# Optimization experiments

Measured on AMD Instinct MI355X. Metric: run time of the kernel, lower is better.

The kernel has to match this reference:

```python
import jax, jax.numpy as jnp
import numpy as np
from jax import lax

B_CAPS, C_CAPS, K, STRIDE, ITERS = 32, 32, 3, 2, 3
BATCH, WIN = 8, 14
W_OUT = (WIN - K) // STRIDE + 1  # 6
CWW = C_CAPS * W_OUT * W_OUT     # 1152
LOG_2PI = float(np.log(2.0 * np.pi))


def setup_inputs() -> dict:
    key = jax.random.key(0)
    k1, k2, k3, k4, k5 = jax.random.split(key, 5)
    return {
        "poses": jax.random.normal(k1, (BATCH, B_CAPS, WIN, WIN, 16), jnp.float32),
        "activations": jax.random.uniform(k2, (BATCH, B_CAPS, WIN, WIN), jnp.float32),
        "lambda_": jnp.ones((), jnp.float32),
        "W": jax.random.normal(k3, (B_CAPS, K, K, C_CAPS, 4, 4), jnp.float32),
        "beta_v": jax.random.normal(k4, (1, CWW, 1), jnp.float32),
        "beta_a": jax.random.normal(k5, (1, CWW), jnp.float32),
    }


def reference(poses, activations, lambda_, W, beta_v, beta_a):
    b, B, win = poses.shape[0], poses.shape[1], poses.shape[2]
    C = W.shape[3]
    w = (win - K) // STRIDE + 1
    Bkk, Cww = B * K * K, C * w * w

    pose = poses.reshape(b, 16, B, win, win).transpose(0, 2, 3, 4, 1)

    # im2col patch extraction (vectorized): rows[i,k] = stride*i + k
    rows = ((jnp.arange(w) * STRIDE)[:, None] + jnp.arange(K)).reshape(-1)  # (w*K,)
    p = jnp.take(pose, rows, axis=2).reshape(b, B, w, K, win, 16)
    p = jnp.take(p, rows, axis=4).reshape(b, B, w, K, w, K, 16)
    patches = p.transpose(0, 1, 3, 5, 6, 2, 4)          # (b,B,K,K,16,wi,wj)
    # faithful reproduction of torch's view (b,B,K,K,16,ww)->(b,B,K,K,1,w,w,4,4)
    patches = patches.reshape(b, B, K, K, w, w, 4, 4)

    # votes: broadcast 4x4 matmul W @ pose-patch
    votes = jnp.einsum('sxyzij,bsxyuvjk->bsxyzuvik', W, patches)
    votes = votes.reshape(b, Bkk, Cww, 16)

    # activation patches, tiled over C (coordinate_add=False branch)
    a = jnp.take(activations, rows, axis=2).reshape(b, B, w, K, win)
    a = jnp.take(a, rows, axis=4).reshape(b, B, w, K, w, K)
    a = a.transpose(0, 1, 3, 5, 2, 4).reshape(b, Bkk, 1, w * w)
    act = jnp.broadcast_to(a, (b, Bkk, C, w * w)).reshape(b, Bkk, Cww)

    # EM routing
    R = jnp.ones((b, Bkk, Cww), votes.dtype) / Cww
    for i in range(ITERS + 1):
        Ra = (R * act)[..., None]                        # (b,Bkk,Cww,1)
        sum_R = Ra.sum(1)                                # (b,Cww,1)
        mu = ((Ra * votes).sum(1) / sum_R)[:, None]      # (b,1,Cww,16)
        sigma_sq = (Ra * (votes - mu) ** 2).sum(1) / sum_R  # (b,Cww,16)
        if i != ITERS:
            mu_d = lax.stop_gradient(mu)
            ss_d = lax.stop_gradient(sigma_sq)[:, None]  # (b,1,Cww,16)
            V_d = lax.stop_gradient(votes)
            a_d = lax.stop_gradient(act)
            log_p = -0.5 * (V_d - mu_d) ** 2 / ss_d - 0.5 * jnp.log(ss_d) - 0.5 * LOG_2PI
            ap = a_d * jnp.exp(log_p).sum(-1)            # (b,Bkk,Cww)
            R = ap / ap.sum(-1, keepdims=True)
        else:
            cost = (beta_v + jnp.log(sigma_sq)) * sum_R  # (b,Cww,16)
            a_out = jax.nn.sigmoid(lambda_ * (beta_a - cost.sum(2)))  # (b,Cww)

    return (mu.reshape(b, C, w, w, 16), a_out.reshape(b, C, w, w))
```

## Files before the change

kernel.cpp:

```cpp
#include <hip/hip_runtime.h>
#include <hip/hip_bf16.h>

#define NB   8
#define NM   288
#define NN   1152
#define NUV  36
#define ND   16

#define OFF_P    0
#define SZ_P     (NB*NUV*NM*ND)
#define OFF_WT   (OFF_P + SZ_P)
#define SZ_WT    (32*NM*ND)
#define OFF_ACT  (OFF_WT + SZ_WT)
#define SZ_ACT   (NB*NUV*NM)
#define OFF_L    (OFF_ACT + SZ_ACT)
#define SZ_L     (NB*NN*NM)
#define OFF_LSE  (OFF_L + SZ_L)
#define SZ_LSE   (NB*NM)
#define OFF_FLAG (OFF_LSE + SZ_LSE)
#define OFF_PM   (OFF_FLAG + 16)
#define SZ_PM    (NB*NUV*NM)
#define OFF_PS   (OFF_PM + SZ_PM)
#define SZ_PS    (NB*NUV*NM)

#define HALF_LOG_2PI 0.9189385332046727f
#define LOG_NN       7.049254841255839f
#define NEG_BIG      (-1.0e30f)

__device__ __forceinline__ float ldin(const void* p, int i, int f32) {
    return f32 ? ((const float*)p)[i]
               : __bfloat162float(((const __hip_bfloat16*)p)[i]);
}

__device__ __forceinline__ unsigned short bfbits(float f) {
    __hip_bfloat16 h = __float2bfloat16(f);
    return __builtin_bit_cast(unsigned short, h);
}

__device__ __forceinline__ float dot2bf(unsigned a, unsigned b, float c) {
    float d;
    asm("v_dot2_f32_bf16 %0, %1, %2, %3" : "=v"(d) : "v"(a), "v"(b), "v"(c));
    return d;
}

__device__ __forceinline__ int sniff(const unsigned short* u16) {
    int wild = 0;
    for (int i = 0; i < 64; ++i) {
        int ex = (u16[i] >> 7) & 0xFF;
        if (ex >= 133) ++wild;
    }
    return (wild >= 4) ? 1 : 0;
}

__global__ __launch_bounds__(256) void prep_kernel(
    const void* __restrict__ poses, const void* __restrict__ acts,
    const void* __restrict__ Wb, __hip_bfloat16* __restrict__ P,
    __hip_bfloat16* __restrict__ Wt, float* __restrict__ A36,
    int* __restrict__ flagw)
{
    const int blk = blockIdx.x;
    const int tid = threadIdx.x;
    __shared__ int lflag;
    if (tid == 0) {
        int f = sniff((const unsigned short*)poses);
        lflag = f;
        if (blk == 0) *flagw = f;
    }
    __syncthreads();
    const int f32 = lflag;

    if (blk < 256) {
        __shared__ float ps[16 * 196];
        __shared__ float asld[196];
        const int b = blk >> 5, s = blk & 31;
        for (int e = tid; e < 16 * 196; e += 256) {
            int c = e / 196, hw = e % 196;
            ps[e] = ldin(poses, ((b * 16 + c) * 32 + s) * 196 + hw, f32);
        }
        for (int e = tid; e < 196; e += 256)
            asld[e] = ldin(acts, (b * 32 + s) * 196 + e, f32);
        __syncthreads();
        for (int o2 = tid; o2 < 648; o2 += 256) {
            int row = o2 >> 1, half = o2 & 1;
            int uv = row / 9, xy = row % 9;
            int u = uv / 6, vv2 = uv % 6;
            int x = xy / 3, y = xy % 3;
            unsigned pk[4];
#pragma unroll
            for (int h = 0; h < 4; ++h) {
                unsigned lohi[2];
#pragma unroll
                for (int e = 0; e < 2; ++e) {
                    int kj = half * 8 + h * 2 + e;
                    int k = kj >> 2, j = kj & 3;
                    int idx = u * 96 + vv2 * 16 + j * 4 + k;
                    int c = idx / 36, rem = idx % 36;
                    int wi = rem / 6, wj = rem % 6;
                    lohi[e] = bfbits(ps[c * 196 + (2 * wi + x) * 14 + (2 * wj + y)]);
                }
                pk[h] = lohi[0] | (lohi[1] << 16);
            }
            *((uint4*)(P + (((size_t)((b * 36 + uv) * 288 + s * 9 + xy)) << 4) + half * 8)) =
                make_uint4(pk[0], pk[1], pk[2], pk[3]);
        }
        for (int o = tid; o < 324; o += 256) {
            int uv = o / 9, xy = o % 9;
            int u = uv / 6, vv2 = uv % 6;
            int x = xy / 3, y = xy % 3;
            A36[(b * 36 + uv) * 288 + s * 9 + xy] =
                __logf(asld[(2 * u + x) * 14 + (2 * vv2 + y)]);
        }
    } else {
        int idx = (blk - 256) * 256 + tid;
        int z = idx / 288, m = idx % 288;
        unsigned pk[8];
#pragma unroll
        for (int h = 0; h < 8; ++h) {
            unsigned lo = bfbits(ldin(Wb, m * 512 + z * 16 + 2 * h, f32));
            unsigned hi = bfbits(ldin(Wb, m * 512 + z * 16 + 2 * h + 1, f32));
            pk[h] = lo | (hi << 16);
        }
        uint4* dst = (uint4*)(Wt + idx * 16);
        dst[0] = make_uint4(pk[0], pk[1], pk[2], pk[3]);
        dst[1] = make_uint4(pk[4], pk[5], pk[6], pk[7]);
    }
}

__global__ __launch_bounds__(288, 4) void em_iter(
    const unsigned short* __restrict__ wsP, const unsigned short* __restrict__ wsWt,
    const float* __restrict__ wsA, float* __restrict__ wsL,
    const float* __restrict__ wsLSE,
    const void* __restrict__ beta_v,
    const void* __restrict__ beta_a,
    const void* __restrict__ lambda_,
    void* __restrict__ outv, const int* __restrict__ flagp, int iter)
{
    __shared__ float red[NM * 17];
    __shared__ float paru[NM];
    __shared__ float parv[NM];
    __shared__ float paruW[18];
    __shared__ float mul[16], nhil[16], ltl[16], ssl[16];

    const int tid = threadIdx.x;
    const int B   = blockIdx.x;
    const int rr  = B & 255;
    const int z   = rr >> 3;
    const int g   = ((B >> 8) << 3) | (rr & 7);
    const int b   = g / NUV;
    const int uv  = g % NUV;
    const int n   = z * NUV + uv;
    const int bn  = b * NN + n;

    const uint4* Wq = (const uint4*)(wsWt + ((z * NM + tid) << 4));
    const uint4* Pq = (const uint4*)(wsP + ((g * NM + tid) << 4));
    uint4 wq0 = Wq[0], wq1 = Wq[1];
    uint4 pq0 = Pq[0], pq1 = Pq[1];
    const float lact = wsA[g * NM + tid];
    float t;
    if (iter == 0) t = lact - LOG_NN;
    else t = wsL[(size_t)bn * NM + tid] - wsLSE[b * NM + tid] + lact;
    t = fmaxf(t, NEG_BIG);

    const float w = __expf(t);

    unsigned Wa[4]  = {wq0.x, wq0.z, wq1.x, wq1.z};
    unsigned Wb_[4] = {wq0.y, wq0.w, wq1.y, wq1.w};
    unsigned Pa[4]  = {pq0.x, pq0.z, pq1.x, pq1.z};
    unsigned Pb[4]  = {pq0.y, pq0.w, pq1.y, pq1.w};
    float v[16];
#pragma unroll
    for (int i = 0; i < 4; ++i)
#pragma unroll
        for (int k = 0; k < 4; ++k)
            v[i * 4 + k] = dot2bf(Wa[i], Pa[k], dot2bf(Wb_[i], Pb[k], 0.f));

#pragma unroll
    for (int dd = 0; dd < 16; ++dd) red[tid * 17 + dd] = v[dd];
    red[tid * 17 + 16] = w;
    __syncthreads();

    {
        const int d = tid & 15, c = tid >> 4;
        const float* base = &red[(c << 4) * 17];
        float s1 = 0.f, s2 = 0.f, sw = 0.f;
#pragma unroll
        for (int q = 0; q < 16; ++q) {
            float ww = base[q * 17 + 16];
            float vv = base[q * 17 + d];
            float t1 = ww * vv;
            s1 += t1; s2 += t1 * vv; sw += ww;
        }
        paru[d * 18 + c] = s1;
        parv[d * 18 + c] = s2;
        if (d == 0) paruW[c] = sw;
    }
    __syncthreads();

    float sW_f = 0.f;
    if (tid < 16) {
        float sW = 0.f, S1 = 0.f, S2 = 0.f;
#pragma unroll
        for (int c = 0; c < 18; ++c) {
            sW += paruW[c];
            S1 += paru[tid * 18 + c];
            S2 += parv[tid * 18 + c];
        }
        float mu = S1 / sW;
        float q2 = S2 / sW;
        float ss = fmaxf(q2 - mu * mu, 1e-30f);
        mul[tid]  = mu;
        ssl[tid]  = ss;
        nhil[tid] = -0.5f / ss;
        ltl[tid]  = fmaf(-0.5f, __logf(ss), -HALF_LOG_2PI);
        sW_f = sW;
    }
    __syncthreads();

    if (iter < 3) {
        float lp[16];
        float M = NEG_BIG;
#pragma unroll
        for (int dd = 0; dd < 16; ++dd) {
            float df = v[dd] - mul[dd];
            lp[dd] = fmaf(df * df, nhil[dd], ltl[dd]);
            M = fmaxf(M, lp[dd]);
        }
        float s = 0.f;
#pragma unroll
        for (int dd = 0; dd < 16; ++dd) s += __expf(lp[dd] - M);
        wsL[(size_t)bn * NM + tid] = lact + M + __logf(s);
    } else {
        const int f32 = *flagp;
        if (tid < 16) {
            if (f32) ((float*)outv)[(bn << 4) + tid] = mul[tid];
            else ((__hip_bfloat16*)outv)[(bn << 4) + tid] = __float2bfloat16(mul[tid]);
        }
        if (tid == 0) {
            float sumR = sW_f;
            float bv = ldin(beta_v, n, f32);
            float c = 0.f;
#pragma unroll
            for (int dd = 0; dd < 16; ++dd) c += bv + __logf(ssl[dd]);
            c *= sumR;
            float lam = ldin(lambda_, 0, f32);
            float ba  = ldin(beta_a, n, f32);
            float ao  = 1.f / (1.f + __expf(-(lam * (ba - c))));
            int oi = NB * NN * ND + bn;
            if (f32) ((float*)outv)[oi] = ao;
            else ((__hip_bfloat16*)outv)[oi] = __float2bfloat16(ao);
        }
    }
}

__global__ __launch_bounds__(288) void lse1_kernel(const float* __restrict__ L,
                                                   float* __restrict__ PM,
                                                   float* __restrict__ PS)
{
    const int tid = threadIdx.x;
    const int blk = blockIdx.x;
    const int b = blk / NUV;
    const int c = blk % NUV;
    const float* base = L + ((size_t)b * NN + c * 32) * NM + tid;
    float mx = NEG_BIG;
#pragma unroll
    for (int r = 0; r < 32; ++r) mx = fmaxf(mx, base[r * NM]);
    float s = 0.f;
#pragma unroll
    for (int r = 0; r < 32; ++r) s += __expf(base[r * NM] - mx);
    PM[blk * NM + tid] = mx;
    PS[blk * NM + tid] = s;
}

__global__ void lse2_kernel(const float* __restrict__ PM,
                            const float* __restrict__ PS,
                            float* __restrict__ LSE)
{
    int t = blockIdx.x * 256 + threadIdx.x;
    if (t >= NB * NM) return;
    int b = t / NM, m = t % NM;
    const float* pm = PM + (size_t)b * NUV * NM + m;
    const float* ps = PS + (size_t)b * NUV * NM + m;
    float mx = NEG_BIG;
#pragma unroll
    for (int cc = 0; cc < NUV; ++cc) mx = fmaxf(mx, pm[cc * NM]);
    float s = 0.f;
#pragma unroll
    for (int cc = 0; cc < NUV; ++cc) s += ps[cc * NM] * __expf(pm[cc * NM] - mx);
    LSE[t] = mx + __logf(s);
}

extern "C" void kernel_launch(void* const* d_in, const int* in_sizes, int n_in,
                              void* d_out, int out_size, void* d_ws, size_t ws_size,
                              hipStream_t stream)
{
    const void* poses = d_in[0];
    const void* acts  = d_in[1];
    const void* lam   = d_in[2];
    const void* Wb    = d_in[3];
    const void* bv    = d_in[4];
    const void* ba    = d_in[5];

    float* ws  = (float*)d_ws;
    __hip_bfloat16* P  = (__hip_bfloat16*)(ws + OFF_P);
    __hip_bfloat16* Wt = (__hip_bfloat16*)(ws + OFF_WT);
    float* A36 = ws + OFF_ACT;
    float* L   = ws + OFF_L;
    float* LSE = ws + OFF_LSE;
    int*  flag = (int*)(ws + OFF_FLAG);
    float* PM  = ws + OFF_PM;
    float* PS  = ws + OFF_PS;

    prep_kernel<<<292, 256, 0, stream>>>(poses, acts, Wb, P, Wt, A36, flag);

    for (int it = 0; it < 4; ++it) {
        em_iter<<<NB * NN, 288, 0, stream>>>((const unsigned short*)P,
                                             (const unsigned short*)Wt,
                                             A36, L, LSE, bv, ba, lam,
                                             d_out, flag, it);
        if (it < 3) {
            lse1_kernel<<<NB * NUV, 288, 0, stream>>>(L, PM, PS);
            lse2_kernel<<<9, 256, 0, stream>>>(PM, PS, LSE);
        }
    }
}
```

Before: 214.4 us.

## Replace log-space LSE reduction kernels with linear-domain atomic row sums

Routing weights move from log space back to the linear domain. Each em_iter block now accumulates the per-(batch, input capsule) normalisation sum with atomicAdd into a per-iteration buffer that prep_kernel zeroes. This removes the two LSE reduction kernels launched per iteration, their extra passes over L, and some exp/log work. The cost is 9216 blocks x 288 atomics per iteration, non-deterministic summation order, and possible underflow or overflow, since the max-subtraction stabilisation is gone.

```diff
diff --git a/kernel.cpp b/kernel.cpp
--- a/kernel.cpp
+++ b/kernel.cpp
@@ -15,17 +15,12 @@
 #define SZ_ACT   (NB*NUV*NM)
 #define OFF_L    (OFF_ACT + SZ_ACT)
 #define SZ_L     (NB*NN*NM)
-#define OFF_LSE  (OFF_L + SZ_L)
-#define SZ_LSE   (NB*NM)
-#define OFF_FLAG (OFF_LSE + SZ_LSE)
-#define OFF_PM   (OFF_FLAG + 16)
-#define SZ_PM    (NB*NUV*NM)
-#define OFF_PS   (OFF_PM + SZ_PM)
-#define SZ_PS    (NB*NUV*NM)
+#define OFF_S    (OFF_L + SZ_L)
+#define SZ_S     (3*NB*NM)
+#define OFF_FLAG (OFF_S + SZ_S)
 
 #define HALF_LOG_2PI 0.9189385332046727f
-#define LOG_NN       7.049254841255839f
-#define NEG_BIG      (-1.0e30f)
+#define INV_NN       (1.0f/1152.0f)
 
 __device__ __forceinline__ float ldin(const void* p, int i, int f32) {
     return f32 ? ((const float*)p)[i]
@@ -56,7 +51,7 @@
     const void* __restrict__ poses, const void* __restrict__ acts,
     const void* __restrict__ Wb, __hip_bfloat16* __restrict__ P,
     __hip_bfloat16* __restrict__ Wt, float* __restrict__ A36,
-    int* __restrict__ flagw)
+    float* __restrict__ S, int* __restrict__ flagw)
 {
     const int blk = blockIdx.x;
     const int tid = threadIdx.x;
@@ -108,10 +103,11 @@
             int u = uv / 6, vv2 = uv % 6;
             int x = xy / 3, y = xy % 3;
             A36[(b * 36 + uv) * 288 + s * 9 + xy] =
-                __logf(asld[(2 * u + x) * 14 + (2 * vv2 + y)]);
+                asld[(2 * u + x) * 14 + (2 * vv2 + y)];
         }
     } else {
         int idx = (blk - 256) * 256 + tid;
+        if (idx < 3 * NB * NM) S[idx] = 0.f;
         int z = idx / 288, m = idx % 288;
         unsigned pk[8];
 #pragma unroll
@@ -129,7 +125,7 @@
 __global__ __launch_bounds__(288, 4) void em_iter(
     const unsigned short* __restrict__ wsP, const unsigned short* __restrict__ wsWt,
     const float* __restrict__ wsA, float* __restrict__ wsL,
-    const float* __restrict__ wsLSE,
+    float* __restrict__ wsS,
     const void* __restrict__ beta_v,
     const void* __restrict__ beta_a,
     const void* __restrict__ lambda_,
@@ -155,13 +151,15 @@
     const uint4* Pq = (const uint4*)(wsP + ((g * NM + tid) << 4));
     uint4 wq0 = Wq[0], wq1 = Wq[1];
     uint4 pq0 = Pq[0], pq1 = Pq[1];
-    const float lact = wsA[g * NM + tid];
-    float t;
-    if (iter == 0) t = lact - LOG_NN;
-    else t = wsL[(size_t)bn * NM + tid] - wsLSE[b * NM + tid] + lact;
-    t = fmaxf(t, NEG_BIG);
-
-    const float w = __expf(t);
+    const float act = wsA[g * NM + tid];
+    float w;
+    if (iter == 0) {
+        w = act * INV_NN;
+    } else {
+        float Ap = wsL[(size_t)bn * NM + tid];
+        float Sv = wsS[(iter - 1) * (NB * NM) + b * NM + tid];
+        w = Ap * act / Sv;
+    }
 
     unsigned Wa[4]  = {wq0.x, wq0.z, wq1.x, wq1.z};
     unsigned Wb_[4] = {wq0.y, wq0.w, wq1.y, wq1.w};
@@ -217,18 +215,15 @@
     __syncthreads();
 
     if (iter < 3) {
-        float lp[16];
-        float M = NEG_BIG;
+        float s = 0.f;
 #pragma unroll
         for (int dd = 0; dd < 16; ++dd) {
             float df = v[dd] - mul[dd];
-            lp[dd] = fmaf(df * df, nhil[dd], ltl[dd]);
-            M = fmaxf(M, lp[dd]);
-        }
-        float s = 0.f;
-#pragma unroll
-        for (int dd = 0; dd < 16; ++dd) s += __expf(lp[dd] - M);
-        wsL[(size_t)bn * NM + tid] = lact + M + __logf(s);
+            s += __expf(fmaf(df * df, nhil[dd], ltl[dd]));
+        }
+        float Aval = act * s;
+        wsL[(size_t)bn * NM + tid] = Aval;
+        atomicAdd(&wsS[iter * (NB * NM) + b * NM + tid], Aval);
     } else {
         const int f32 = *flagp;
         if (tid < 16) {
@@ -250,43 +245,6 @@
             else ((__hip_bfloat16*)outv)[oi] = __float2bfloat16(ao);
         }
     }
-}
-
-__global__ __launch_bounds__(288) void lse1_kernel(const float* __restrict__ L,
-                                                   float* __restrict__ PM,
-                                                   float* __restrict__ PS)
-{
-    const int tid = threadIdx.x;
-    const int blk = blockIdx.x;
-    const int b = blk / NUV;
-    const int c = blk % NUV;
-    const float* base = L + ((size_t)b * NN + c * 32) * NM + tid;
-    float mx = NEG_BIG;
-#pragma unroll
-    for (int r = 0; r < 32; ++r) mx = fmaxf(mx, base[r * NM]);
-    float s = 0.f;
-#pragma unroll
-    for (int r = 0; r < 32; ++r) s += __expf(base[r * NM] - mx);
-    PM[blk * NM + tid] = mx;
-    PS[blk * NM + tid] = s;
-}
-
-__global__ void lse2_kernel(const float* __restrict__ PM,
-                            const float* __restrict__ PS,
-                            float* __restrict__ LSE)
-{
-    int t = blockIdx.x * 256 + threadIdx.x;
-    if (t >= NB * NM) return;
-    int b = t / NM, m = t % NM;
-    const float* pm = PM + (size_t)b * NUV * NM + m;
-    const float* ps = PS + (size_t)b * NUV * NM + m;
-    float mx = NEG_BIG;
-#pragma unroll
-    for (int cc = 0; cc < NUV; ++cc) mx = fmaxf(mx, pm[cc * NM]);
-    float s = 0.f;
-#pragma unroll
-    for (int cc = 0; cc < NUV; ++cc) s += ps[cc * NM] * __expf(pm[cc * NM] - mx);
-    LSE[t] = mx + __logf(s);
 }
 
 extern "C" void kernel_launch(void* const* d_in, const int* in_sizes, int n_in,
@@ -305,21 +263,15 @@
     __hip_bfloat16* Wt = (__hip_bfloat16*)(ws + OFF_WT);
     float* A36 = ws + OFF_ACT;
     float* L   = ws + OFF_L;
-    float* LSE = ws + OFF_LSE;
+    float* S   = ws + OFF_S;
     int*  flag = (int*)(ws + OFF_FLAG);
-    float* PM  = ws + OFF_PM;
-    float* PS  = ws + OFF_PS;
-
-    prep_kernel<<<292, 256, 0, stream>>>(poses, acts, Wb, P, Wt, A36, flag);
+
+    prep_kernel<<<292, 256, 0, stream>>>(poses, acts, Wb, P, Wt, A36, S, flag);
 
     for (int it = 0; it < 4; ++it) {
         em_iter<<<NB * NN, 288, 0, stream>>>((const unsigned short*)P,
                                              (const unsigned short*)Wt,
-                                             A36, L, LSE, bv, ba, lam,
+                                             A36, L, S, bv, ba, lam,
                                              d_out, flag, it);
-        if (it < 3) {
-            lse1_kernel<<<NB * NUV, 288, 0, stream>>>(L, PM, PS);
-            lse2_kernel<<<9, 256, 0, stream>>>(PM, PS, LSE);
-        }
-    }
-}
+    }
+}
```

Result: slower. 327.0 us (+52.5%).
